# Kernel optimization log

Hardware: AMD Instinct MI355X
Metric: run time of the kernel (lower is better)

## Reference

```python
import jax, jax.numpy as jnp
import numpy as np

N, E, IN, H0, H1 = 50000, 1600000, 64, 64, 128


def _gcn(h, W, b, row, col):
    # PyG GCNConv, add_self_loops=False, unit edge weights:
    # out[col] += d^{-1/2}[row] * d^{-1/2}[col] * (h @ W)[row]; bias added after aggregation
    n = h.shape[0]
    deg = jnp.zeros((n,), h.dtype).at[col].add(jnp.ones((row.shape[0],), h.dtype))
    dinv = jnp.where(deg > 0, jax.lax.rsqrt(jnp.maximum(deg, 1e-12)), 0.0)
    norm = (dinv[row] * dinv[col])[:, None]  # [E,1]
    m = h @ W  # transform before propagate (small GEMM)
    out = jnp.zeros((n, W.shape[1]), h.dtype).at[col].add(norm * m[row])
    return out + b


def _bn(h, g, b):
    # BatchNorm1d training-mode math (biased variance), eps=1e-5
    mu = h.mean(0)
    var = ((h - mu) ** 2).mean(0)
    return g * (h - mu) * jax.lax.rsqrt(var + 1e-5) + b


def _san(h):
    return jnp.nan_to_num(h, nan=0.0, posinf=100.0, neginf=-100.0)


def _slice(x, ei, W0, b0, W1, b1, res1, g0, be0, g1, be1):
    row, col = ei[0], ei[1]
    # layer 0: conv -> bn -> relu -> (dropout=eval identity) -> residual (Identity, 64==64) -> nan_to_num
    h1 = _san(jax.nn.relu(_bn(_gcn(x, W0, b0, row, col), g0, be0)) + x)
    # layer 1 (last): conv -> bn -> residual (Linear proj 64->128, no bias) -> nan_to_num
    h2 = _san(_bn(_gcn(h1, W1, b1, row, col), g1, be1) + h1 @ res1)
    return h2


def setup_inputs() -> dict:
    k = jax.random.split(jax.random.key(0), 16)
    f = lambda kk, sh, s: jax.random.normal(kk, sh, jnp.float32) * s
    return {
        "x": f(k[0], (N, IN), 1.0),
        "edge_index0": jax.random.randint(k[1], (2, E), 0, N),
        "edge_index1": jax.random.randint(k[2], (2, E), 0, N),
        "w0_s0": f(k[3], (IN, H0), 0.1), "b0_s0": jnp.zeros((H0,), jnp.float32),
        "w1_s0": f(k[4], (H0, H1), 0.1), "b1_s0": jnp.zeros((H1,), jnp.float32),
        "res1_s0": f(k[5], (H0, H1), 0.1),
        "w0_s1": f(k[6], (IN, H0), 0.1), "b0_s1": jnp.zeros((H0,), jnp.float32),
        "w1_s1": f(k[7], (H0, H1), 0.1), "b1_s1": jnp.zeros((H1,), jnp.float32),
        "res1_s1": f(k[8], (H0, H1), 0.1),
        "bn_g0": jnp.ones((H0,), jnp.float32), "bn_b0": jnp.zeros((H0,), jnp.float32),
        "bn_g1": jnp.ones((H1,), jnp.float32), "bn_b1": jnp.zeros((H1,), jnp.float32),
        "fc1_w": f(k[9], (2 * H1, H1), 0.1), "fc1_b": jnp.zeros((H1,), jnp.float32),
        "fc2_w": f(k[10], (H1, 2), 0.1), "fc2_b": jnp.zeros((2,), jnp.float32),
    }


def reference(x, edge_index0, edge_index1,
              w0_s0, b0_s0, w1_s0, b1_s0, res1_s0,
              w0_s1, b0_s1, w1_s1, b1_s1, res1_s1,
              bn_g0, bn_b0, bn_g1, bn_b1,
              fc1_w, fc1_b, fc2_w, fc2_b):
    out0 = _slice(x, edge_index0, w0_s0, b0_s0, w1_s0, b1_s0, res1_s0, bn_g0, bn_b0, bn_g1, bn_b1)
    out1 = _slice(x, edge_index1, w0_s1, b0_s1, w1_s1, b1_s1, res1_s1, bn_g0, bn_b0, bn_g1, bn_b1)
    combined = jnp.concatenate([out0, out1], axis=1)  # [N, 2*H1]
    h = jax.nn.relu(combined @ fc1_w + fc1_b)  # dropout is eval-mode identity
    logits = h @ fc2_w + fc2_b
    return logits, jax.nn.softmax(logits, axis=1)
```

## Files before the change

kernel.cpp:

```cpp
#include <hip/hip_runtime.h>
#include <hip/hip_bf16.h>
#include <math.h>


typedef short v8s __attribute__((ext_vector_type(8)));
typedef float f32x4 __attribute__((ext_vector_type(4)));

#define BSTRIDE 10240

__device__ __forceinline__ float sanf(float v) {
    if (v != v) return 0.f;
    if (isinf(v)) return v > 0.f ? 100.f : -100.f;
    return v;
}

__device__ __forceinline__ unsigned short bf16of(float v) {
    __hip_bfloat16 h = __float2bfloat16(v);
    return *(unsigned short*)&h;
}
__device__ __forceinline__ unsigned pack2(float lo, float hi) {
    return (unsigned)bf16of(lo) | ((unsigned)bf16of(hi) << 16);
}
__device__ __forceinline__ float uflo(unsigned u) { return __uint_as_float(u << 16); }
__device__ __forceinline__ float ufhi(unsigned u) { return __uint_as_float(u & 0xFFFF0000u); }

__device__ __forceinline__ void packone(const float* __restrict__ src, unsigned* __restrict__ dst,
                                        int L, int Khalf, int F) {
    int c = L / Khalf, kp = L - c * Khalf;
    dst[L] = pack2(src[(2 * kp) * F + c], src[(2 * kp + 1) * F + c]);
}

__global__ __launch_bounds__(256) void prep_kernel(const float* __restrict__ w0_0,
                                                   const float* __restrict__ w0_1,
                                                   const float* __restrict__ w1_0,
                                                   const float* __restrict__ w1_1,
                                                   const float* __restrict__ r_0,
                                                   const float* __restrict__ r_1,
                                                   const float* __restrict__ fc1,
                                                   unsigned* __restrict__ wpk,
                                                   int* __restrict__ bcnt,
                                                   float* __restrict__ sums) {
    int gid = blockIdx.x * 256 + threadIdx.x;
    if (gid < 512) bcnt[gid] = 0;
    if (gid < 8192) sums[gid] = 0.f;
    if (gid < 2048)       packone(w0_0, wpk + 0,     gid - 0,     32, 64);
    else if (gid < 4096)  packone(w0_1, wpk + 2048,  gid - 2048,  32, 64);
    else if (gid < 8192)  packone(w1_0, wpk + 4096,  gid - 4096,  32, 128);
    else if (gid < 12288) packone(w1_1, wpk + 8192,  gid - 8192,  32, 128);
    else if (gid < 16384) packone(r_0,  wpk + 12288, gid - 12288, 32, 128);
    else if (gid < 20480) packone(r_1,  wpk + 16384, gid - 16384, 32, 128);
    else if (gid < 36864) packone(fc1,  wpk + 20480, gid - 20480, 128, 128);
}


__global__ __launch_bounds__(512) void kC_bin(const int* __restrict__ ei0,
                                              const int* __restrict__ ei1,
                                              int* __restrict__ bcnt,
                                              unsigned* __restrict__ binned,
                                              int E, int n) {
    __shared__ int cnt[512];
    __shared__ int base[512];
    int t = threadIdx.x;
    cnt[t] = 0;
    int E2 = 2 * E;
    int e0 = blockIdx.x * 8192;
    unsigned pk[16];
    int bk[16];
    __syncthreads();
#pragma unroll
    for (int j = 0; j < 16; ++j) {
        int ge = e0 + t + j * 512;
        bk[j] = -1;
        if (ge < E2) {
            int slice = ge >= E;
            const int* ei = slice ? ei1 : ei0;
            int e = ge - slice * E;
            int col = ei[E + e], row = ei[e];
            int gcol = slice * n + col;
            bk[j] = gcol >> 8;
            pk[j] = (unsigned)row | (((unsigned)gcol & 255u) << 16);
            atomicAdd(&cnt[bk[j]], 1);
        }
    }
    __syncthreads();
    {
        int c = cnt[t];
        base[t] = c ? atomicAdd(&bcnt[t], c) : 0;
    }
    __syncthreads();
    cnt[t] = 0;
    __syncthreads();
#pragma unroll
    for (int j = 0; j < 16; ++j) {
        if (bk[j] >= 0) {
            int loc = atomicAdd(&cnt[bk[j]], 1);
            int off = base[bk[j]] + loc;
            if (off < BSTRIDE) binned[(size_t)bk[j] * BSTRIDE + off] = pk[j];
        }
    }
}

__global__ __launch_bounds__(512) void kD_build(const unsigned* __restrict__ binned,
                                                const int* __restrict__ bcnt,
                                                const float* __restrict__ x,
                                                int* __restrict__ rowptr,
                                                float* __restrict__ dinv,
                                                unsigned short* __restrict__ csr,
                                                unsigned short* __restrict__ xsb,
                                                int n2, int NB) {
    __shared__ int pref[512];
    __shared__ int cnt[256];
    __shared__ int scn[256];
    __shared__ int cur[256];
    __shared__ float ds[256];
    int b = blockIdx.x, t = threadIdx.x;
    int n = n2 >> 1, n64 = n * 64;
    pref[t] = (t < NB) ? bcnt[t] : 0;
    __syncthreads();
    for (int off = 1; off < 512; off <<= 1) {
        int u = (t >= off) ? pref[t - off] : 0;
        __syncthreads();
        pref[t] += u;
        __syncthreads();
    }
    int s = (b > 0) ? pref[b - 1] : 0;
    int e = pref[b];
    int m = e - s;
    const unsigned* seg = binned + (size_t)b * BSTRIDE;
    if (t < 256) cnt[t] = 0;
    __syncthreads();
    for (int i = t; i < m; i += 512) atomicAdd(&cnt[(seg[i] >> 16) & 255], 1);
    __syncthreads();
    int v = (t < 256) ? cnt[t] : 0;
    if (t < 256) scn[t] = v;
    __syncthreads();
    for (int off = 1; off < 256; off <<= 1) {
        int u = (t < 256 && t >= off) ? scn[t - off] : 0;
        __syncthreads();
        if (t < 256) scn[t] += u;
        __syncthreads();
    }
    if (t < 256) {
        int excl = scn[t] - v;
        int gcol = b * 256 + t;
        float dv = v > 0 ? rsqrtf((float)v) : 0.f;
        ds[t] = dv;
        if (gcol < n2) {
            rowptr[gcol] = s + excl;
            dinv[gcol] = dv;
        }
        cur[t] = excl;
    }
    __syncthreads();
    for (int i = t; i < m; i += 512) {
        unsigned p = seg[i];
        int cl = (p >> 16) & 255;
        int pos = s + atomicAdd(&cur[cl], 1);
        csr[pos] = (unsigned short)(p & 0xFFFFu);
    }
    if (b == NB - 1 && t == 0) rowptr[n2] = e;
    for (int k = t; k < 2048; k += 512) {
        int gl = k >> 3, segk = k & 7;
        int gcol = b * 256 + gl;
        if (gcol >= n2) continue;
        float d = ds[gl];
        int slice = gcol >= n;
        int row = gcol - slice * n;
        const float* xp = x + (size_t)row * 64 + segk * 8;
        float4 v0 = *(const float4*)xp;
        float4 v1 = *(const float4*)(xp + 4);
        uint4 o;
        o.x = pack2(v0.x * d, v0.y * d); o.y = pack2(v0.z * d, v0.w * d);
        o.z = pack2(v1.x * d, v1.y * d); o.w = pack2(v1.z * d, v1.w * d);
        *(uint4*)&xsb[(size_t)slice * n64 + (size_t)row * 64 + segk * 8] = o;
    }
}


#define LOAD8(U, IDX)                                                       \
    do {                                                                    \
        _Pragma("unroll") for (int j = 0; j < 8; ++j) {                     \
            int r = __shfl((IDX), j, 8);                                    \
            (U)[j] = *(const uint4*)&mb[(size_t)r * 64 + l * 8];            \
        }                                                                   \
    } while (0)
#define ZPAD8(U, BB)                                                        \
    do {                                                                    \
        _Pragma("unroll") for (int j = 0; j < 8; ++j)                       \
            if ((BB) + j >= e) { (U)[j].x = 0; (U)[j].y = 0;                \
                                 (U)[j].z = 0; (U)[j].w = 0; }              \
    } while (0)
#define ACC8(U)                                                             \
    do {                                                                    \
        _Pragma("unroll") for (int j = 0; j < 8; ++j) {                     \
            a0 += uflo((U)[j].x); a1 += ufhi((U)[j].x);                     \
            a2 += uflo((U)[j].y); a3 += ufhi((U)[j].y);                     \
            a4 += uflo((U)[j].z); a5 += ufhi((U)[j].z);                     \
            a6 += uflo((U)[j].w); a7 += ufhi((U)[j].w);                     \
        }                                                                   \
    } while (0)

__global__ __launch_bounds__(256) void gatherbf_kernel(const int* __restrict__ rowptr,
                                                       const unsigned short* __restrict__ csr,
                                                       const unsigned short* __restrict__ xsb,
                                                       const float* __restrict__ dinv,
                                                       unsigned short* __restrict__ outb,
                                                       int n) {
    int blk = blockIdx.x;
    int xcd = blk & 7;
    int slice = (xcd >= 4) ? 1 : 0;
    int rank = (blk >> 3) * 4 + (xcd & 3);
    int nodeLocal = rank * 32 + (threadIdx.x >> 3);
    if (nodeLocal >= n) return;
    int node = slice * n + nodeLocal;
    int l = threadIdx.x & 7;
    const unsigned short* mb = xsb + (size_t)slice * n * 64;
    int s = rowptr[node], e = rowptr[node + 1];
    float a0 = 0.f, a1 = 0.f, a2 = 0.f, a3 = 0.f, a4 = 0.f, a5 = 0.f, a6 = 0.f, a7 = 0.f;
    uint4 uA[8], uB[8];
    int b = s;
    if (b + 8 <= e) {
        int ia = csr[b + l];
        LOAD8(uA, ia);
        int bB = b + 8;
        int ib = (bB + l < e) ? (int)csr[bB + l] : 0;
        while (true) {
            bool hasB = (bB < e);
            if (hasB) {
                LOAD8(uB, ib);
                if (bB + 8 > e) ZPAD8(uB, bB);
            }
            int bA2 = bB + 8;
            if (bA2 < e) ia = (bA2 + l < e) ? (int)csr[bA2 + l] : 0;
            ACC8(uA);
            if (!hasB) break;
            bool hasA2 = (bA2 < e);
            if (hasA2) {
                LOAD8(uA, ia);
                if (bA2 + 8 > e) ZPAD8(uA, bA2);
            }
            int bB2 = bA2 + 8;
            if (bB2 < e) ib = (bB2 + l < e) ? (int)csr[bB2 + l] : 0;
            ACC8(uB);
            if (!hasA2) break;
            bB = bB2;
        }
    } else if (b < e) {
        int ia = (b + l < e) ? (int)csr[b + l] : 0;
        LOAD8(uA, ia);
        ZPAD8(uA, b);
        ACC8(uA);
    }
    float d = dinv[node];
    uint4 o;
    o.x = pack2(a0 * d, a1 * d);
    o.y = pack2(a2 * d, a3 * d);
    o.z = pack2(a4 * d, a5 * d);
    o.w = pack2(a6 * d, a7 * d);
    *(uint4*)&outb[(size_t)node * 64 + l * 8] = o;
}

__global__ __launch_bounds__(256) void mfma_gemmb64(const unsigned short* __restrict__ Ab,
                                                    const unsigned* __restrict__ WT0,
                                                    const unsigned* __restrict__ WT1,
                                                    unsigned short* __restrict__ Cb,
                                                    float* __restrict__ sums_base,
                                                    int roff, int n) {
    constexpr int F = 64;
    constexpr int NC = F / 16;
    __shared__ float ls[2 * F];
    __shared__ unsigned short stb[64 * F];
    int BPS = (n + 63) >> 6;
    int slice = blockIdx.x >= BPS;
    int sb = blockIdx.x - slice * BPS;
    const unsigned* WT = slice ? WT1 : WT0;
    int row0 = slice * n + sb * 64;
    int rows = min(64, n - sb * 64);
    for (int i = threadIdx.x; i < 2 * F; i += 256) ls[i] = 0.f;
    int w = threadIdx.x >> 6, lane = threadIdx.x & 63, q = lane >> 4, ln = lane & 15;
    const unsigned* A32 = (const unsigned*)Ab;
    size_t arow = (size_t)(row0 + 16 * w + ln) * 32;
    v8s af0 = *(const v8s*)&A32[arow + q * 4];
    v8s af1 = *(const v8s*)&A32[arow + 16 + q * 4];
    f32x4 acc[NC];
#pragma unroll
    for (int ct = 0; ct < NC; ++ct) acc[ct] = {0.f, 0.f, 0.f, 0.f};
#pragma unroll
    for (int ct = 0; ct < NC; ++ct) {
        v8s b0 = *(const v8s*)&WT[(ct * 16 + ln) * 32 + q * 4];
        v8s b1 = *(const v8s*)&WT[(ct * 16 + ln) * 32 + 16 + q * 4];
        acc[ct] = __builtin_amdgcn_mfma_f32_16x16x32_bf16(af0, b0, acc[ct], 0, 0, 0);
        acc[ct] = __builtin_amdgcn_mfma_f32_16x16x32_bf16(af1, b1, acc[ct], 0, 0, 0);
    }
    __syncthreads();
#pragma unroll
    for (int ct = 0; ct < NC; ++ct) {
        float s1 = 0.f, s2 = 0.f;
        int cc = ct * 16 + ln;
#pragma unroll
        for (int i = 0; i < 4; ++i) {
            int r = 16 * w + q * 4 + i;
            stb[r * F + (cc ^ ((r & 7) << 3))] = bf16of(acc[ct][i]);
            if (r < rows) {
                float v = acc[ct][i];
                s1 += v;
                s2 += v * v;
            }
        }
        s1 += __shfl_xor(s1, 16); s1 += __shfl_xor(s1, 32);
        s2 += __shfl_xor(s2, 16); s2 += __shfl_xor(s2, 32);
        if (q == 0) {
            atomicAdd(&ls[cc], s1);
            atomicAdd(&ls[F + cc], s2);
        }
    }
    __syncthreads();
    {
        constexpr int CPT = F / 4;
        int rr = threadIdx.x >> 2, sg = threadIdx.x & 3;
        if (rr < rows) {
            int swz = (rr & 7) << 3;
            int cb = sg * CPT;
            uint4* dst = (uint4*)(Cb + (size_t)(row0 + rr) * F + cb);
#pragma unroll
            for (int jj = 0; jj < CPT / 8; ++jj)
                dst[jj] = *(const uint4*)&stb[rr * F + ((cb + jj * 8) ^ swz)];
        }
    }
    if (threadIdx.x < F) {
        float* dst = sums_base + (blockIdx.x & 7) * 1024 + roff + slice * 2 * F;
        unsafeAtomicAdd(&dst[threadIdx.x], ls[threadIdx.x]);
        unsafeAtomicAdd(&dst[F + threadIdx.x], ls[F + threadIdx.x]);
    }
}

__global__ __launch_bounds__(256) void mfma_gemmb128f(const unsigned short* __restrict__ Ab,
                                                      const unsigned* __restrict__ WT0,
                                                      const unsigned* __restrict__ WT1,
                                                      unsigned short* __restrict__ Tfrag,
                                                      float* __restrict__ sums_base,
                                                      int n) {
    __shared__ float ls[256];
    int BPS = (n + 63) >> 6;
    int slice = blockIdx.x >= BPS;
    int sb = blockIdx.x - slice * BPS;
    const unsigned* WT = slice ? WT1 : WT0;
    int row0 = slice * n + sb * 64;
    int rows = min(64, n - sb * 64);
    for (int i = threadIdx.x; i < 256; i += 256) ls[i] = 0.f;
    int w = threadIdx.x >> 6, lane = threadIdx.x & 63, q = lane >> 4, ln = lane & 15;
    const unsigned* A32 = (const unsigned*)Ab;
    size_t arow = (size_t)(row0 + 16 * w + ln) * 32;
    v8s af0 = *(const v8s*)&A32[arow + q * 4];
    v8s af1 = *(const v8s*)&A32[arow + 16 + q * 4];
    f32x4 acc[8];
#pragma unroll
    for (int ct = 0; ct < 8; ++ct) acc[ct] = {0.f, 0.f, 0.f, 0.f};
#pragma unroll
    for (int ct = 0; ct < 8; ++ct) {
        v8s b0 = *(const v8s*)&WT[(ct * 16 + ln) * 32 + q * 4];
        v8s b1 = *(const v8s*)&WT[(ct * 16 + ln) * 32 + 16 + q * 4];
        acc[ct] = __builtin_amdgcn_mfma_f32_16x16x32_bf16(af0, b0, acc[ct], 0, 0, 0);
        acc[ct] = __builtin_amdgcn_mfma_f32_16x16x32_bf16(af1, b1, acc[ct], 0, 0, 0);
    }
    __syncthreads();
    unsigned short* tb = Tfrag + (size_t)blockIdx.x * 8192;
#pragma unroll
    for (int ct = 0; ct < 8; ++ct) {
        uint2 o2;
        o2.x = pack2(acc[ct][0], acc[ct][1]);
        o2.y = pack2(acc[ct][2], acc[ct][3]);
        *(uint2*)&tb[((ct * 4 + w) * 64 + lane) * 4] = o2;
        float s1 = 0.f, s2 = 0.f;
        int cc = ct * 16 + ln;
#pragma unroll
        for (int i = 0; i < 4; ++i) {
            int r = 16 * w + q * 4 + i;
            if (r < rows) {
                float v = acc[ct][i];
                s1 += v;
                s2 += v * v;
            }
        }
        s1 += __shfl_xor(s1, 16); s1 += __shfl_xor(s1, 32);
        s2 += __shfl_xor(s2, 16); s2 += __shfl_xor(s2, 32);
        if (q == 0) {
            atomicAdd(&ls[cc], s1);
            atomicAdd(&ls[128 + cc], s2);
        }
    }
    __syncthreads();
    if (threadIdx.x < 128) {
        float* dst = sums_base + (blockIdx.x & 7) * 1024 + slice * 256;
        unsafeAtomicAdd(&dst[threadIdx.x], ls[threadIdx.x]);
        unsafeAtomicAdd(&dst[128 + threadIdx.x], ls[128 + threadIdx.x]);
    }
}

__global__ __launch_bounds__(256) void apply0_kernel(const unsigned short* __restrict__ t0b,
                                                     const float* __restrict__ x,
                                                     const float* __restrict__ sums_base,
                                                     const float* __restrict__ g,
                                                     const float* __restrict__ be,
                                                     const float* __restrict__ dinv,
                                                     unsigned short* __restrict__ h1b,
                                                     unsigned short* __restrict__ h1sb,
                                                     int n64, int total, int n) {
    __shared__ float sc[256];
    int t = threadIdx.x;
    if (t < 128) {
        int slice = t >> 6, f = t & 63;
        float s1 = 0.f, s2 = 0.f;
#pragma unroll
        for (int r = 0; r < 8; ++r) {
            const float* src = sums_base + r * 1024 + 512 + slice * 128;
            s1 += src[f];
            s2 += src[64 + f];
        }
        float inv_n = 1.0f / (float)n;
        float mu = s1 * inv_n;
        float var = fmaxf(s2 * inv_n - mu * mu, 0.f);
        float scale = g[f] * rsqrtf(var + 1e-5f);
        sc[slice * 128 + f] = scale;
        sc[slice * 128 + 64 + f] = be[f] - mu * scale;
    }
    __syncthreads();
    int i8 = (blockIdx.x * 256 + t) * 8;
    if (i8 >= total) return;
    int slice = i8 >= n64;
    int f0 = i8 & 63;
    const float* scp = sc + slice * 128;
    uint4 tv = *(const uint4*)&t0b[i8];
    const float* xp = x + (i8 - slice * n64);
    float4 x0 = *(const float4*)xp;
    float4 x1 = *(const float4*)(xp + 4);
    float4 s0 = *(const float4*)&scp[f0];
    float4 s1 = *(const float4*)&scp[f0 + 4];
    float4 g0 = *(const float4*)&scp[64 + f0];
    float4 g1 = *(const float4*)&scp[64 + f0 + 4];
    float d = dinv[i8 >> 6];
    float tvv[8] = {uflo(tv.x), ufhi(tv.x), uflo(tv.y), ufhi(tv.y),
                    uflo(tv.z), ufhi(tv.z), uflo(tv.w), ufhi(tv.w)};
    float sa[8] = {s0.x, s0.y, s0.z, s0.w, s1.x, s1.y, s1.z, s1.w};
    float sh[8] = {g0.x, g0.y, g0.z, g0.w, g1.x, g1.y, g1.z, g1.w};
    float xv[8] = {x0.x, x0.y, x0.z, x0.w, x1.x, x1.y, x1.z, x1.w};
    unsigned po[4], ps[4];
#pragma unroll
    for (int j = 0; j < 4; ++j) {
        float a = sanf(fmaxf(fmaf(tvv[2 * j], sa[2 * j], sh[2 * j]), 0.f) + xv[2 * j]);
        float b = sanf(fmaxf(fmaf(tvv[2 * j + 1], sa[2 * j + 1], sh[2 * j + 1]), 0.f) + xv[2 * j + 1]);
        po[j] = pack2(a, b);
        ps[j] = pack2(a * d, b * d);
    }
    *(uint4*)&h1b[i8] = *(uint4*)po;
    *(uint4*)&h1sb[i8] = *(uint4*)ps;
}

__global__ __launch_bounds__(256) void apply1_head(const unsigned short* __restrict__ h1b,
                                                   const unsigned short* __restrict__ Tfrag,
                                                   const unsigned* __restrict__ RT0,
                                                   const unsigned* __restrict__ RT1,
                                                   const unsigned* __restrict__ FT,
                                                   const float* __restrict__ sums_base,
                                                   const float* __restrict__ g,
                                                   const float* __restrict__ be,
                                                   const float* __restrict__ fc1_b,
                                                   const float* __restrict__ w2,
                                                   const float* __restrict__ b2,
                                                   float* __restrict__ out, int n) {
    __shared__ unsigned short cmb[64 * 256];
    __shared__ float scl[512];
    int t = threadIdx.x;
    int BPS = (n + 63) >> 6;
    int row0l = blockIdx.x * 64;
    int rows = min(64, n - row0l);
    {
        int slice = t >> 7, f = t & 127;
        float s1 = 0.f, s2 = 0.f;
#pragma unroll
        for (int r = 0; r < 8; ++r) {
            const float* src = sums_base + r * 1024 + slice * 256;
            s1 += src[f];
            s2 += src[128 + f];
        }
        float inv_n = 1.0f / (float)n;
        float mu = s1 * inv_n;
        float var = fmaxf(s2 * inv_n - mu * mu, 0.f);
        float scale = g[f] * rsqrtf(var + 1e-5f);
        scl[slice * 256 + f] = scale;
        scl[slice * 256 + 128 + f] = be[f] - mu * scale;
    }
    __syncthreads();
    int w = t >> 6, lane = t & 63, q = lane >> 4, ln = lane & 15;
    int rbase = 16 * w + q * 4;
#pragma unroll
    for (int slice = 0; slice < 2; ++slice) {
        const unsigned* WT = slice ? RT1 : RT0;
        int row0 = slice * n + row0l;
        const unsigned* A32 = (const unsigned*)h1b;
        size_t arow = (size_t)(row0 + 16 * w + ln) * 32;
        v8s af0 = *(const v8s*)&A32[arow + q * 4];
        v8s af1 = *(const v8s*)&A32[arow + 16 + q * 4];
        f32x4 acc[8];
#pragma unroll
        for (int ct = 0; ct < 8; ++ct) acc[ct] = {0.f, 0.f, 0.f, 0.f};
#pragma unroll
        for (int ct = 0; ct < 8; ++ct) {
            v8s b0 = *(const v8s*)&WT[(ct * 16 + ln) * 32 + q * 4];
            v8s b1 = *(const v8s*)&WT[(ct * 16 + ln) * 32 + 16 + q * 4];
            acc[ct] = __builtin_amdgcn_mfma_f32_16x16x32_bf16(af0, b0, acc[ct], 0, 0, 0);
            acc[ct] = __builtin_amdgcn_mfma_f32_16x16x32_bf16(af1, b1, acc[ct], 0, 0, 0);
        }
        const unsigned short* tb = Tfrag + (size_t)(slice * BPS + blockIdx.x) * 8192;
        const float* scb = scl + slice * 256;
#pragma unroll
        for (int ct = 0; ct < 8; ++ct) {
            uint2 tf = *(const uint2*)&tb[((ct * 4 + w) * 64 + lane) * 4];
            int c = ct * 16 + ln;
            float sc_ = scb[c], sh_ = scb[128 + c];
            float o0 = sanf(fmaf(uflo(tf.x), sc_, sh_) + acc[ct][0]);
            float o1 = sanf(fmaf(ufhi(tf.x), sc_, sh_) + acc[ct][1]);
            float o2 = sanf(fmaf(uflo(tf.y), sc_, sh_) + acc[ct][2]);
            float o3 = sanf(fmaf(ufhi(tf.y), sc_, sh_) + acc[ct][3]);
            int gc = slice * 128 + c;
            cmb[(rbase + 0) * 256 + (gc ^ (((rbase + 0) & 7) << 3))] = bf16of(o0);
            cmb[(rbase + 1) * 256 + (gc ^ (((rbase + 1) & 7) << 3))] = bf16of(o1);
            cmb[(rbase + 2) * 256 + (gc ^ (((rbase + 2) & 7) << 3))] = bf16of(o2);
            cmb[(rbase + 3) * 256 + (gc ^ (((rbase + 3) & 7) << 3))] = bf16of(o3);
        }
    }
    __syncthreads();
    {
        int rowLocal = 16 * w + ln;
        const unsigned short* cr = cmb + rowLocal * 256;
        int swzR = (rowLocal & 7) << 3;
        f32x4 acc[8];
#pragma unroll
        for (int ct = 0; ct < 8; ++ct) acc[ct] = {0.f, 0.f, 0.f, 0.f};
#pragma unroll
        for (int kt = 0; kt < 4; ++kt) {
            v8s af0 = *(const v8s*)&cr[(kt * 64 + q * 8) ^ swzR];
            v8s af1 = *(const v8s*)&cr[(kt * 64 + 32 + q * 8) ^ swzR];
#pragma unroll
            for (int ct = 0; ct < 8; ++ct) {
                v8s b0 = *(const v8s*)&FT[(ct * 16 + ln) * 128 + kt * 32 + q * 4];
                v8s b1 = *(const v8s*)&FT[(ct * 16 + ln) * 128 + kt * 32 + 16 + q * 4];
                acc[ct] = __builtin_amdgcn_mfma_f32_16x16x32_bf16(af0, b0, acc[ct], 0, 0, 0);
                acc[ct] = __builtin_amdgcn_mfma_f32_16x16x32_bf16(af1, b1, acc[ct], 0, 0, 0);
            }
        }
        float p0[4] = {0.f, 0.f, 0.f, 0.f}, p1[4] = {0.f, 0.f, 0.f, 0.f};
#pragma unroll
        for (int ct = 0; ct < 8; ++ct) {
            int c = ct * 16 + ln;
            float bi = fc1_b[c];
            float w20 = w2[c * 2], w21 = w2[c * 2 + 1];
#pragma unroll
            for (int i = 0; i < 4; ++i) {
                float h = fmaxf(acc[ct][i] + bi, 0.f);
                p0[i] = fmaf(h, w20, p0[i]);
                p1[i] = fmaf(h, w21, p1[i]);
            }
        }
#pragma unroll
        for (int i = 0; i < 4; ++i) {
#pragma unroll
            for (int msk = 1; msk < 16; msk <<= 1) {
                p0[i] += __shfl_xor(p0[i], msk);
                p1[i] += __shfl_xor(p1[i], msk);
            }
        }
        if (ln == 0) {
            float bb0 = b2[0], bb1 = b2[1];
#pragma unroll
            for (int i = 0; i < 4; ++i) {
                int r = 16 * w + q * 4 + i;
                if (r >= rows) continue;
                int R = row0l + r;
                float l0 = p0[i] + bb0, l1 = p1[i] + bb1;
                float mx = fmaxf(l0, l1);
                float e0 = expf(l0 - mx), e1 = expf(l1 - mx);
                float inv = 1.0f / (e0 + e1);
                out[(size_t)R * 2] = l0;
                out[(size_t)R * 2 + 1] = l1;
                out[(size_t)2 * n + R * 2] = e0 * inv;
                out[(size_t)2 * n + R * 2 + 1] = e1 * inv;
            }
        }
    }
}

static inline int cdiv(int a, int b) { return (a + b - 1) / b; }

extern "C" void kernel_launch(void* const* d_in, const int* in_sizes, int n_in,
                              void* d_out, int out_size, void* d_ws, size_t ws_size,
                              hipStream_t stream) {
    const float* x       = (const float*)d_in[0];
    const int*   ei0     = (const int*)d_in[1];
    const int*   ei1     = (const int*)d_in[2];
    const float* w0_s0   = (const float*)d_in[3];
    const float* w1_s0   = (const float*)d_in[5];
    const float* res1_s0 = (const float*)d_in[7];
    const float* w0_s1   = (const float*)d_in[8];
    const float* w1_s1   = (const float*)d_in[10];
    const float* res1_s1 = (const float*)d_in[12];
    const float* bn_g0   = (const float*)d_in[13];
    const float* bn_b0   = (const float*)d_in[14];
    const float* bn_g1   = (const float*)d_in[15];
    const float* bn_b1   = (const float*)d_in[16];
    const float* fc1_w   = (const float*)d_in[17];
    const float* fc1_b   = (const float*)d_in[18];
    const float* fc2_w   = (const float*)d_in[19];
    const float* fc2_b   = (const float*)d_in[20];
    float* out = (float*)d_out;

    int n = in_sizes[0] / 64;
    int E = in_sizes[1] / 2;
    int n2 = 2 * n, E2 = 2 * E;
    int n64 = n * 64;
    int NB = cdiv(n2, 256);
    int BPS = cdiv(n, 64);
    int GB = 8 * cdiv(cdiv(n, 32), 4);

    float* X1 = (float*)d_ws;
    float* S  = X1 + (size_t)2 * BPS * 4096;
    unsigned short* Gb   = (unsigned short*)(S + (size_t)n2 * 64);
    unsigned short* h1b  = Gb + (size_t)n2 * 64;
    unsigned short* comb = h1b + (size_t)n2 * 64;
    unsigned short* xsb  = comb + (size_t)n * 256;
    float* dinv = (float*)(xsb + (size_t)n * 128);
    float* sums = dinv + n2;
    float* scsh = sums + 8192;
    unsigned* wpk = (unsigned*)(scsh + 512);
    unsigned short* csr = (unsigned short*)(wpk + 36864);
    int* rowptr = (int*)(csr + (size_t)E2);
    int* bcnt   = rowptr + (n2 + 1);
    unsigned short* t0b = (unsigned short*)X1;
    unsigned short* Tfrag = (unsigned short*)X1;
    unsigned* binned = (unsigned*)comb;
    unsigned short* h1sb = (unsigned short*)S;
    unsigned* w0T0 = wpk + 0,    *w0T1 = wpk + 2048;
    unsigned* w1T0 = wpk + 4096, *w1T1 = wpk + 8192;
    unsigned* rT0  = wpk + 12288,*rT1  = wpk + 16384;
    unsigned* fT   = wpk + 20480;

    prep_kernel<<<144, 256, 0, stream>>>(w0_s0, w0_s1, w1_s0, w1_s1,
                                         res1_s0, res1_s1, fc1_w, wpk, bcnt, sums);
    kC_bin<<<cdiv(E2, 8192), 512, 0, stream>>>(ei0, ei1, bcnt, binned, E, n);
    kD_build<<<NB, 512, 0, stream>>>(binned, bcnt, x, rowptr, dinv, csr, xsb, n2, NB);

    gatherbf_kernel<<<GB, 256, 0, stream>>>(rowptr, csr, xsb, dinv, Gb, n);
    mfma_gemmb64<<<2 * BPS, 256, 0, stream>>>(Gb, w0T0, w0T1, t0b, sums, 512, n);
    apply0_kernel<<<cdiv(2 * n64, 2048), 256, 0, stream>>>(t0b, x, sums, bn_g0, bn_b0,
                                                           dinv, h1b, h1sb, n64, 2 * n64, n);

    gatherbf_kernel<<<GB, 256, 0, stream>>>(rowptr, csr, h1sb, dinv, Gb, n);
    mfma_gemmb128f<<<2 * BPS, 256, 0, stream>>>(Gb, w1T0, w1T1, Tfrag, sums, n);

    apply1_head<<<BPS, 256, 0, stream>>>(h1b, Tfrag, rT0, rT1, fT, sums, bn_g1, bn_b1,
                                         fc1_b, fc2_w, fc2_b, out, n);
}
```

Before: 342.8 us.

## Split fused apply1+head kernel into per-slice apply and separate FC head

The fused final kernel, which handled both slices and the FC head in one block, is split in two. The first kernel runs one block per slice and row tile, finishing the residual projection, BN and sanitisation, and writes the combined bf16 features to a global buffer. The second kernel reads that buffer and runs the fc1/ReLU/fc2/softmax head. This doubles the block count for the first stage and cuts per-block LDS, aimed at better occupancy and latency hiding. The cost is an extra kernel launch and a round trip of the N×256 bf16 intermediate through global memory.

```diff
diff --git a/kernel.cpp b/kernel.cpp
--- a/kernel.cpp
+++ b/kernel.cpp
@@ -456,136 +456,147 @@
     *(uint4*)&h1sb[i8] = *(uint4*)ps;
 }
 
-__global__ __launch_bounds__(256) void apply1_head(const unsigned short* __restrict__ h1b,
+__global__ __launch_bounds__(256) void apply1_frag(const unsigned short* __restrict__ h1b,
                                                    const unsigned short* __restrict__ Tfrag,
                                                    const unsigned* __restrict__ RT0,
                                                    const unsigned* __restrict__ RT1,
-                                                   const unsigned* __restrict__ FT,
                                                    const float* __restrict__ sums_base,
                                                    const float* __restrict__ g,
                                                    const float* __restrict__ be,
-                                                   const float* __restrict__ fc1_b,
-                                                   const float* __restrict__ w2,
-                                                   const float* __restrict__ b2,
-                                                   float* __restrict__ out, int n) {
-    __shared__ unsigned short cmb[64 * 256];
-    __shared__ float scl[512];
+                                                   unsigned short* __restrict__ comb, int n) {
+    __shared__ unsigned short stb[64 * 128];
+    __shared__ float scl[256];
     int t = threadIdx.x;
     int BPS = (n + 63) >> 6;
-    int row0l = blockIdx.x * 64;
+    int slice = blockIdx.x >= BPS;
+    int sb = blockIdx.x - slice * BPS;
+    int row0l = sb * 64;
     int rows = min(64, n - row0l);
-    {
-        int slice = t >> 7, f = t & 127;
+    if (t < 128) {
         float s1 = 0.f, s2 = 0.f;
 #pragma unroll
         for (int r = 0; r < 8; ++r) {
             const float* src = sums_base + r * 1024 + slice * 256;
-            s1 += src[f];
-            s2 += src[128 + f];
+            s1 += src[t];
+            s2 += src[128 + t];
         }
         float inv_n = 1.0f / (float)n;
         float mu = s1 * inv_n;
         float var = fmaxf(s2 * inv_n - mu * mu, 0.f);
-        float scale = g[f] * rsqrtf(var + 1e-5f);
-        scl[slice * 256 + f] = scale;
-        scl[slice * 256 + 128 + f] = be[f] - mu * scale;
-    }
-    __syncthreads();
+        float scale = g[t] * rsqrtf(var + 1e-5f);
+        scl[t] = scale;
+        scl[128 + t] = be[t] - mu * scale;
+    }
     int w = t >> 6, lane = t & 63, q = lane >> 4, ln = lane & 15;
+    int row0 = slice * n + row0l;
+    const unsigned* WT = slice ? RT1 : RT0;
+    const unsigned* A32 = (const unsigned*)h1b;
+    size_t arow = (size_t)(row0 + 16 * w + ln) * 32;
+    v8s af0 = *(const v8s*)&A32[arow + q * 4];
+    v8s af1 = *(const v8s*)&A32[arow + 16 + q * 4];
+    f32x4 acc[8];
+#pragma unroll
+    for (int ct = 0; ct < 8; ++ct) acc[ct] = {0.f, 0.f, 0.f, 0.f};
+#pragma unroll
+    for (int ct = 0; ct < 8; ++ct) {
+        v8s b0 = *(const v8s*)&WT[(ct * 16 + ln) * 32 + q * 4];
+        v8s b1 = *(const v8s*)&WT[(ct * 16 + ln) * 32 + 16 + q * 4];
+        acc[ct] = __builtin_amdgcn_mfma_f32_16x16x32_bf16(af0, b0, acc[ct], 0, 0, 0);
+        acc[ct] = __builtin_amdgcn_mfma_f32_16x16x32_bf16(af1, b1, acc[ct], 0, 0, 0);
+    }
+    __syncthreads();
+    const unsigned short* tb = Tfrag + (size_t)blockIdx.x * 8192;
     int rbase = 16 * w + q * 4;
 #pragma unroll
-    for (int slice = 0; slice < 2; ++slice) {
-        const unsigned* WT = slice ? RT1 : RT0;
-        int row0 = slice * n + row0l;
-        const unsigned* A32 = (const unsigned*)h1b;
-        size_t arow = (size_t)(row0 + 16 * w + ln) * 32;
-        v8s af0 = *(const v8s*)&A32[arow + q * 4];
-        v8s af1 = *(const v8s*)&A32[arow + 16 + q * 4];
-        f32x4 acc[8];
-#pragma unroll
-        for (int ct = 0; ct < 8; ++ct) acc[ct] = {0.f, 0.f, 0.f, 0.f};
+    for (int ct = 0; ct < 8; ++ct) {
+        uint2 tf = *(const uint2*)&tb[((ct * 4 + w) * 64 + lane) * 4];
+        int c = ct * 16 + ln;
+        float sc_ = scl[c], sh_ = scl[128 + c];
+        float o0 = sanf(fmaf(uflo(tf.x), sc_, sh_) + acc[ct][0]);
+        float o1 = sanf(fmaf(ufhi(tf.x), sc_, sh_) + acc[ct][1]);
+        float o2 = sanf(fmaf(uflo(tf.y), sc_, sh_) + acc[ct][2]);
+        float o3 = sanf(fmaf(ufhi(tf.y), sc_, sh_) + acc[ct][3]);
+        stb[(rbase + 0) * 128 + (c ^ (((rbase + 0) & 7) << 3))] = bf16of(o0);
+        stb[(rbase + 1) * 128 + (c ^ (((rbase + 1) & 7) << 3))] = bf16of(o1);
+        stb[(rbase + 2) * 128 + (c ^ (((rbase + 2) & 7) << 3))] = bf16of(o2);
+        stb[(rbase + 3) * 128 + (c ^ (((rbase + 3) & 7) << 3))] = bf16of(o3);
+    }
+    __syncthreads();
+    {
+        int rr = t >> 2, sg = t & 3;
+        if (rr < rows) {
+            int swz = (rr & 7) << 3;
+            int cb = sg * 32;
+            uint4* dst = (uint4*)(comb + (size_t)(row0l + rr) * 256 + slice * 128 + cb);
+#pragma unroll
+            for (int jj = 0; jj < 4; ++jj)
+                dst[jj] = *(const uint4*)&stb[rr * 128 + ((cb + jj * 8) ^ swz)];
+        }
+    }
+}
+
+__global__ __launch_bounds__(256) void mfma_head_fc2(const unsigned short* __restrict__ comb,
+                                                     const unsigned* __restrict__ FT,
+                                                     const float* __restrict__ bias,
+                                                     const float* __restrict__ w2,
+                                                     const float* __restrict__ b2,
+                                                     float* __restrict__ out, int n) {
+    int row0 = blockIdx.x * 64;
+    int rows = min(64, n - row0);
+    int w = threadIdx.x >> 6, lane = threadIdx.x & 63, q = lane >> 4, ln = lane & 15;
+    const unsigned* A32 = (const unsigned*)comb;
+    size_t arow = (size_t)(row0 + 16 * w + ln) * 128;
+    f32x4 acc[8];
+#pragma unroll
+    for (int ct = 0; ct < 8; ++ct) acc[ct] = {0.f, 0.f, 0.f, 0.f};
+#pragma unroll
+    for (int kt = 0; kt < 4; ++kt) {
+        v8s af0 = *(const v8s*)&A32[arow + kt * 32 + q * 4];
+        v8s af1 = *(const v8s*)&A32[arow + kt * 32 + 16 + q * 4];
 #pragma unroll
         for (int ct = 0; ct < 8; ++ct) {
-            v8s b0 = *(const v8s*)&WT[(ct * 16 + ln) * 32 + q * 4];
-            v8s b1 = *(const v8s*)&WT[(ct * 16 + ln) * 32 + 16 + q * 4];
+            v8s b0 = *(const v8s*)&FT[(ct * 16 + ln) * 128 + kt * 32 + q * 4];
+            v8s b1 = *(const v8s*)&FT[(ct * 16 + ln) * 128 + kt * 32 + 16 + q * 4];
             acc[ct] = __builtin_amdgcn_mfma_f32_16x16x32_bf16(af0, b0, acc[ct], 0, 0, 0);
             acc[ct] = __builtin_amdgcn_mfma_f32_16x16x32_bf16(af1, b1, acc[ct], 0, 0, 0);
         }
-        const unsigned short* tb = Tfrag + (size_t)(slice * BPS + blockIdx.x) * 8192;
-        const float* scb = scl + slice * 256;
-#pragma unroll
-        for (int ct = 0; ct < 8; ++ct) {
-            uint2 tf = *(const uint2*)&tb[((ct * 4 + w) * 64 + lane) * 4];
-            int c = ct * 16 + ln;
-            float sc_ = scb[c], sh_ = scb[128 + c];
-            float o0 = sanf(fmaf(uflo(tf.x), sc_, sh_) + acc[ct][0]);
-            float o1 = sanf(fmaf(ufhi(tf.x), sc_, sh_) + acc[ct][1]);
-            float o2 = sanf(fmaf(uflo(tf.y), sc_, sh_) + acc[ct][2]);
-            float o3 = sanf(fmaf(ufhi(tf.y), sc_, sh_) + acc[ct][3]);
-            int gc = slice * 128 + c;
-            cmb[(rbase + 0) * 256 + (gc ^ (((rbase + 0) & 7) << 3))] = bf16of(o0);
-            cmb[(rbase + 1) * 256 + (gc ^ (((rbase + 1) & 7) << 3))] = bf16of(o1);
-            cmb[(rbase + 2) * 256 + (gc ^ (((rbase + 2) & 7) << 3))] = bf16of(o2);
-            cmb[(rbase + 3) * 256 + (gc ^ (((rbase + 3) & 7) << 3))] = bf16of(o3);
-        }
-    }
-    __syncthreads();
-    {
-        int rowLocal = 16 * w + ln;
-        const unsigned short* cr = cmb + rowLocal * 256;
-        int swzR = (rowLocal & 7) << 3;
-        f32x4 acc[8];
-#pragma unroll
-        for (int ct = 0; ct < 8; ++ct) acc[ct] = {0.f, 0.f, 0.f, 0.f};
-#pragma unroll
-        for (int kt = 0; kt < 4; ++kt) {
-            v8s af0 = *(const v8s*)&cr[(kt * 64 + q * 8) ^ swzR];
-            v8s af1 = *(const v8s*)&cr[(kt * 64 + 32 + q * 8) ^ swzR];
-#pragma unroll
-            for (int ct = 0; ct < 8; ++ct) {
-                v8s b0 = *(const v8s*)&FT[(ct * 16 + ln) * 128 + kt * 32 + q * 4];
-                v8s b1 = *(const v8s*)&FT[(ct * 16 + ln) * 128 + kt * 32 + 16 + q * 4];
-                acc[ct] = __builtin_amdgcn_mfma_f32_16x16x32_bf16(af0, b0, acc[ct], 0, 0, 0);
-                acc[ct] = __builtin_amdgcn_mfma_f32_16x16x32_bf16(af1, b1, acc[ct], 0, 0, 0);
-            }
-        }
-        float p0[4] = {0.f, 0.f, 0.f, 0.f}, p1[4] = {0.f, 0.f, 0.f, 0.f};
-#pragma unroll
-        for (int ct = 0; ct < 8; ++ct) {
-            int c = ct * 16 + ln;
-            float bi = fc1_b[c];
-            float w20 = w2[c * 2], w21 = w2[c * 2 + 1];
-#pragma unroll
-            for (int i = 0; i < 4; ++i) {
-                float h = fmaxf(acc[ct][i] + bi, 0.f);
-                p0[i] = fmaf(h, w20, p0[i]);
-                p1[i] = fmaf(h, w21, p1[i]);
-            }
-        }
+    }
+    float p0[4] = {0.f, 0.f, 0.f, 0.f}, p1[4] = {0.f, 0.f, 0.f, 0.f};
+#pragma unroll
+    for (int ct = 0; ct < 8; ++ct) {
+        int c = ct * 16 + ln;
+        float bi = bias[c];
+        float w20 = w2[c * 2], w21 = w2[c * 2 + 1];
 #pragma unroll
         for (int i = 0; i < 4; ++i) {
-#pragma unroll
-            for (int msk = 1; msk < 16; msk <<= 1) {
-                p0[i] += __shfl_xor(p0[i], msk);
-                p1[i] += __shfl_xor(p1[i], msk);
-            }
-        }
-        if (ln == 0) {
-            float bb0 = b2[0], bb1 = b2[1];
-#pragma unroll
-            for (int i = 0; i < 4; ++i) {
-                int r = 16 * w + q * 4 + i;
-                if (r >= rows) continue;
-                int R = row0l + r;
-                float l0 = p0[i] + bb0, l1 = p1[i] + bb1;
-                float mx = fmaxf(l0, l1);
-                float e0 = expf(l0 - mx), e1 = expf(l1 - mx);
-                float inv = 1.0f / (e0 + e1);
-                out[(size_t)R * 2] = l0;
-                out[(size_t)R * 2 + 1] = l1;
-                out[(size_t)2 * n + R * 2] = e0 * inv;
-                out[(size_t)2 * n + R * 2 + 1] = e1 * inv;
-            }
+            float h = fmaxf(acc[ct][i] + bi, 0.f);
+            p0[i] = fmaf(h, w20, p0[i]);
+            p1[i] = fmaf(h, w21, p1[i]);
+        }
+    }
+#pragma unroll
+    for (int i = 0; i < 4; ++i) {
+#pragma unroll
+        for (int msk = 1; msk < 16; msk <<= 1) {
+            p0[i] += __shfl_xor(p0[i], msk);
+            p1[i] += __shfl_xor(p1[i], msk);
+        }
+    }
+    if (ln == 0) {
+        float bb0 = b2[0], bb1 = b2[1];
+#pragma unroll
+        for (int i = 0; i < 4; ++i) {
+            int r = 16 * w + q * 4 + i;
+            if (r >= rows) continue;
+            int R = row0 + r;
+            float l0 = p0[i] + bb0, l1 = p1[i] + bb1;
+            float mx = fmaxf(l0, l1);
+            float e0 = expf(l0 - mx), e1 = expf(l1 - mx);
+            float inv = 1.0f / (e0 + e1);
+            out[(size_t)R * 2] = l0;
+            out[(size_t)R * 2 + 1] = l1;
+            out[(size_t)2 * n + R * 2] = e0 * inv;
+            out[(size_t)2 * n + R * 2 + 1] = e1 * inv;
         }
     }
 }
@@ -657,6 +668,6 @@
     gatherbf_kernel<<<GB, 256, 0, stream>>>(rowptr, csr, h1sb, dinv, Gb, n);
     mfma_gemmb128f<<<2 * BPS, 256, 0, stream>>>(Gb, w1T0, w1T1, Tfrag, sums, n);
 
-    apply1_head<<<BPS, 256, 0, stream>>>(h1b, Tfrag, rT0, rT1, fT, sums, bn_g1, bn_b1,
-                                         fc1_b, fc2_w, fc2_b, out, n);
-}
+    apply1_frag<<<2 * BPS, 256, 0, stream>>>(h1b, Tfrag, rT0, rT1, sums, bn_g1, bn_b1, comb, n);
+    mfma_head_fc2<<<BPS, 256, 0, stream>>>(comb, fT, fc1_b, fc2_w, fc2_b, out, n);
+}
```

Result: no change. 348.6 us, median of 2 (+1.7%).
